# Optimization experiments

Hardware: AMD Instinct MI355X
Metric: run time of the kernel (lower is better)

## Reference

```python
import jax, jax.numpy as jnp
import numpy as np

RCUT = 6.0
RCUT_SMTH = 0.5


def _smooth_cosine(r):
    # piecewise: 1 for r < rcut_smth; 0.5*cos(pi*u)+0.5 for rcut_smth <= r < rcut; 0 beyond
    u = (r - RCUT_SMTH) / (RCUT - RCUT_SMTH)
    mid = 0.5 * jnp.cos(jnp.float32(np.pi) * u) + 0.5
    return jnp.where(r < RCUT_SMTH, jnp.ones_like(r),
                     jnp.where(r < RCUT, mid, jnp.zeros_like(r)))


def setup_inputs() -> dict:
    key = jax.random.key(0)
    k1, k2 = jax.random.split(key)
    B, F, N = 4, 4, 1024
    coord = jax.random.normal(k1, (B, F, N, 3), dtype=jnp.float32) * 5.0
    atype = jax.random.randint(k2, (B, N), 0, 2, dtype=jnp.int64)
    return {"coord": coord, "atype": atype}


def reference(coord, atype):
    # coord: [B, F, N, 3] -> descriptor [B, F, N*3]
    B, F, N, _ = coord.shape
    # pairwise difference: diff[b,f,i,j,:] = coord[b,f,i] - coord[b,f,j]
    diff = coord[:, :, :, None, :] - coord[:, :, None, :, :]  # [B,F,N,N,3]
    dist = jnp.sqrt(jnp.sum(diff * diff, axis=-1) + 1e-10)     # [B,F,N,N]
    s_ij = _smooth_cosine(dist)                                # [B,F,N,N]
    desc = jnp.sum(s_ij[..., None] * diff, axis=3)             # [B,F,N,3]
    return desc.reshape(B, F, N * 3)
```

## Files before the change

kernel.cpp:

```cpp
#include <hip/hip_runtime.h>


#define NA   1024
#define IPB  16
#define JLEN 64

__global__ __launch_bounds__(256) void desc_kernel(const float* __restrict__ coord,
                                                   float* __restrict__ out) {
    __shared__ float4 s_c[NA];
    __shared__ float  s_red[4][IPB][3];

    const int tid     = threadIdx.x;
    const int blk     = blockIdx.x;
    const int frame   = blk >> 6;
    const int ibk     = blk & 63;
    const int i_local = tid & 15;
    const int jc      = tid >> 4;

    const float* gf = coord + frame * (NA * 3);

    for (int a = tid; a < NA; a += 256) {
        s_c[a] = make_float4(gf[3 * a], gf[3 * a + 1], gf[3 * a + 2], 0.0f);
    }
    __syncthreads();

    const int    i  = ibk * IPB + i_local;
    const float4 ci = s_c[i];
    const float  cx = ci.x, cy = ci.y, cz = ci.z;

    float ax = 0.0f, ay = 0.0f, az = 0.0f;
    const int   jbase = jc * JLEN;
    const float INV11 = 1.0f / 11.0f;
    const float OFF   = -0.5f / 11.0f;

#pragma unroll 8
    for (int t = 0; t < JLEN; ++t) {
        const int    j  = jbase + ((t + jc) & (JLEN - 1));
        const float4 cj = s_c[j];
        const float  dx = cx - cj.x;
        const float  dy = cy - cj.y;
        const float  dz = cz - cj.z;
        const float  d2 = fmaf(dx, dx, fmaf(dy, dy, fmaf(dz, dz, 1e-10f)));
        const float  r  = __builtin_amdgcn_sqrtf(d2);
        float rev = fmaf(r, INV11, OFF);
        rev = fminf(fmaxf(rev, 0.0f), 0.5f);
        const float s = fmaf(0.5f, __builtin_amdgcn_cosf(rev), 0.5f);
        ax = fmaf(s, dx, ax);
        ay = fmaf(s, dy, ay);
        az = fmaf(s, dz, az);
    }

    ax += __shfl_xor(ax, 16, 64); ax += __shfl_xor(ax, 32, 64);
    ay += __shfl_xor(ay, 16, 64); ay += __shfl_xor(ay, 32, 64);
    az += __shfl_xor(az, 16, 64); az += __shfl_xor(az, 32, 64);

    const int wave = tid >> 6;
    if ((tid & 48) == 0) {
        s_red[wave][i_local][0] = ax;
        s_red[wave][i_local][1] = ay;
        s_red[wave][i_local][2] = az;
    }
    __syncthreads();

    if (tid < IPB * 3) {
        const int il   = tid / 3;
        const int comp = tid - il * 3;
        const float v = s_red[0][il][comp] + s_red[1][il][comp] +
                        s_red[2][il][comp] + s_red[3][il][comp];
        out[frame * (NA * 3) + (ibk * IPB + il) * 3 + comp] = v;
    }
}

extern "C" void kernel_launch(void* const* d_in, const int* in_sizes, int n_in,
                              void* d_out, int out_size, void* d_ws, size_t ws_size,
                              hipStream_t stream) {
    const float* coord = (const float*)d_in[0];
    float*       out   = (float*)d_out;
    (void)d_ws; (void)ws_size; (void)n_in; (void)out_size;

    const int frames = in_sizes[0] / (NA * 3);
    const int blocks = frames * (NA / IPB);

    hipLaunchKernelGGL(desc_kernel, dim3(blocks), dim3(256), 0, stream, coord, out);
}
```

Before: 63.32 us.

## Compute two i-atoms per thread, vectorize coord load, pad shared memory

Each thread now handles two i atoms against each loaded j coordinate, so every shared-memory read serves twice the work and the block count is halved. The coordinate staging uses float4 global loads, and the shared array is padded by one entry every 64 atoms so j-chunk bases fall in different banks, replacing the rotated j index. The cost is more registers per thread and fewer blocks in flight, which lowers the parallelism available across the GPU.

```diff
diff --git a/kernel.cpp b/kernel.cpp
--- a/kernel.cpp
+++ b/kernel.cpp
@@ -2,71 +2,92 @@
 
 
 #define NA   1024
-#define IPB  16
+#define IPB  32
+#define NJC  16
 #define JLEN 64
 
 __global__ __launch_bounds__(256) void desc_kernel(const float* __restrict__ coord,
                                                    float* __restrict__ out) {
-    __shared__ float4 s_c[NA];
-    __shared__ float  s_red[4][IPB][3];
+    __shared__ float4 s_c[NA + NA / 64];
+    __shared__ float  s_red[4][16][2][3];
 
-    const int tid     = threadIdx.x;
-    const int blk     = blockIdx.x;
-    const int frame   = blk >> 6;
-    const int ibk     = blk & 63;
-    const int i_local = tid & 15;
-    const int jc      = tid >> 4;
+    const int tid   = threadIdx.x;
+    const int blk   = blockIdx.x;
+    const int frame = blk >> 5;
+    const int ibk   = blk & 31;
+    const int ig    = tid & 15;
+    const int jc    = tid >> 4;
 
-    const float* gf = coord + frame * (NA * 3);
-
-    for (int a = tid; a < NA; a += 256) {
-        s_c[a] = make_float4(gf[3 * a], gf[3 * a + 1], gf[3 * a + 2], 0.0f);
+    const float4* gf4 = (const float4*)(coord + frame * (NA * 3));
+    {
+        const float4 f0 = gf4[3 * tid + 0];
+        const float4 f1 = gf4[3 * tid + 1];
+        const float4 f2 = gf4[3 * tid + 2];
+        const int a0 = 4 * tid;
+        const int p  = a0 + (a0 >> 6);
+        s_c[p + 0] = make_float4(f0.x, f0.y, f0.z, 0.0f);
+        s_c[p + 1] = make_float4(f0.w, f1.x, f1.y, 0.0f);
+        s_c[p + 2] = make_float4(f1.z, f1.w, f2.x, 0.0f);
+        s_c[p + 3] = make_float4(f2.y, f2.z, f2.w, 0.0f);
     }
     __syncthreads();
 
-    const int    i  = ibk * IPB + i_local;
-    const float4 ci = s_c[i];
-    const float  cx = ci.x, cy = ci.y, cz = ci.z;
+    const int    ia  = ibk * IPB + 2 * ig;
+    const int    ip  = ia + (ia >> 6);
+    const float4 ci0 = s_c[ip];
+    const float4 ci1 = s_c[ip + 1];
 
-    float ax = 0.0f, ay = 0.0f, az = 0.0f;
-    const int   jbase = jc * JLEN;
+    const float4* pj = &s_c[65 * jc];
+
+    float ax0 = 0.f, ay0 = 0.f, az0 = 0.f;
+    float ax1 = 0.f, ay1 = 0.f, az1 = 0.f;
     const float INV11 = 1.0f / 11.0f;
     const float OFF   = -0.5f / 11.0f;
 
 #pragma unroll 8
     for (int t = 0; t < JLEN; ++t) {
-        const int    j  = jbase + ((t + jc) & (JLEN - 1));
-        const float4 cj = s_c[j];
-        const float  dx = cx - cj.x;
-        const float  dy = cy - cj.y;
-        const float  dz = cz - cj.z;
-        const float  d2 = fmaf(dx, dx, fmaf(dy, dy, fmaf(dz, dz, 1e-10f)));
-        const float  r  = __builtin_amdgcn_sqrtf(d2);
-        float rev = fmaf(r, INV11, OFF);
-        rev = fminf(fmaxf(rev, 0.0f), 0.5f);
-        const float s = fmaf(0.5f, __builtin_amdgcn_cosf(rev), 0.5f);
-        ax = fmaf(s, dx, ax);
-        ay = fmaf(s, dy, ay);
-        az = fmaf(s, dz, az);
+        const float4 cj = pj[t];
+        {
+            const float dx = ci0.x - cj.x, dy = ci0.y - cj.y, dz = ci0.z - cj.z;
+            const float d2 = fmaf(dx, dx, fmaf(dy, dy, fmaf(dz, dz, 1e-10f)));
+            const float r  = __builtin_amdgcn_sqrtf(d2);
+            float rev = fmaf(r, INV11, OFF);
+            rev = fminf(fmaxf(rev, 0.0f), 0.5f);
+            const float s = fmaf(0.5f, __builtin_amdgcn_cosf(rev), 0.5f);
+            ax0 = fmaf(s, dx, ax0); ay0 = fmaf(s, dy, ay0); az0 = fmaf(s, dz, az0);
+        }
+        {
+            const float dx = ci1.x - cj.x, dy = ci1.y - cj.y, dz = ci1.z - cj.z;
+            const float d2 = fmaf(dx, dx, fmaf(dy, dy, fmaf(dz, dz, 1e-10f)));
+            const float r  = __builtin_amdgcn_sqrtf(d2);
+            float rev = fmaf(r, INV11, OFF);
+            rev = fminf(fmaxf(rev, 0.0f), 0.5f);
+            const float s = fmaf(0.5f, __builtin_amdgcn_cosf(rev), 0.5f);
+            ax1 = fmaf(s, dx, ax1); ay1 = fmaf(s, dy, ay1); az1 = fmaf(s, dz, az1);
+        }
     }
 
-    ax += __shfl_xor(ax, 16, 64); ax += __shfl_xor(ax, 32, 64);
-    ay += __shfl_xor(ay, 16, 64); ay += __shfl_xor(ay, 32, 64);
-    az += __shfl_xor(az, 16, 64); az += __shfl_xor(az, 32, 64);
+    ax0 += __shfl_xor(ax0, 16, 64); ax0 += __shfl_xor(ax0, 32, 64);
+    ay0 += __shfl_xor(ay0, 16, 64); ay0 += __shfl_xor(ay0, 32, 64);
+    az0 += __shfl_xor(az0, 16, 64); az0 += __shfl_xor(az0, 32, 64);
+    ax1 += __shfl_xor(ax1, 16, 64); ax1 += __shfl_xor(ax1, 32, 64);
+    ay1 += __shfl_xor(ay1, 16, 64); ay1 += __shfl_xor(ay1, 32, 64);
+    az1 += __shfl_xor(az1, 16, 64); az1 += __shfl_xor(az1, 32, 64);
 
     const int wave = tid >> 6;
     if ((tid & 48) == 0) {
-        s_red[wave][i_local][0] = ax;
-        s_red[wave][i_local][1] = ay;
-        s_red[wave][i_local][2] = az;
+        s_red[wave][ig][0][0] = ax0; s_red[wave][ig][0][1] = ay0; s_red[wave][ig][0][2] = az0;
+        s_red[wave][ig][1][0] = ax1; s_red[wave][ig][1][1] = ay1; s_red[wave][ig][1][2] = az1;
     }
     __syncthreads();
 
     if (tid < IPB * 3) {
         const int il   = tid / 3;
         const int comp = tid - il * 3;
-        const float v = s_red[0][il][comp] + s_red[1][il][comp] +
-                        s_red[2][il][comp] + s_red[3][il][comp];
+        const int g    = il >> 1;
+        const int ii   = il & 1;
+        const float v = s_red[0][g][ii][comp] + s_red[1][g][ii][comp] +
+                        s_red[2][g][ii][comp] + s_red[3][g][ii][comp];
         out[frame * (NA * 3) + (ibk * IPB + il) * 3 + comp] = v;
     }
 }
```

New measurement: 62.72 us. No clear change (-0.9%).
